# Performance work log

Hardware: AMD Instinct MI355X
Metric: run time of the kernel (lower is better)

The kernel has to match this reference:

```python
import jax, jax.numpy as jnp
import numpy as np

EPS = 1e-5
NUM_HEADS = 12

def _ln(x, g, b):
    m = jnp.mean(x, -1, keepdims=True)
    v = jnp.var(x, -1, keepdims=True)
    return (x - m) * jax.lax.rsqrt(v + EPS) * g + b

def setup_inputs():
    key = jax.random.key(0)
    ks = jax.random.split(key, 8)
    D, Dh = 768, 3072
    B, T, H, Wd = 8, 8, 14, 14
    def w(k, shape, scale=0.02):
        return jax.random.normal(k, shape, jnp.float32) * scale
    return dict(
        x=jax.random.normal(ks[0], (B, T * H * Wd + 1, D), jnp.float32),
        W_mq=w(ks[1], (D, D)), b_mq=jnp.zeros((D,), jnp.float32),
        W_mk=w(ks[2], (D, D)), b_mk=jnp.zeros((D,), jnp.float32),
        g1=jnp.ones((D,), jnp.float32), be1=jnp.zeros((D,), jnp.float32),
        W_qkv=w(ks[3], (3 * D, D)),
        W_proj=w(ks[4], (D, D)), b_proj=jnp.zeros((D,), jnp.float32),
        g2=jnp.ones((D,), jnp.float32), be2=jnp.zeros((D,), jnp.float32),
        W_fc1=w(ks[5], (Dh, D)), b_fc1=jnp.zeros((Dh,), jnp.float32),
        W_fc2=w(ks[6], (D, Dh)), b_fc2=jnp.zeros((D,), jnp.float32),
        B=B, T=T, H=H, Wd=Wd,
    )

def reference(x, W_mq, b_mq, W_mk, b_mk, g1, be1, W_qkv, W_proj, b_proj,
              g2, be2, W_fc1, b_fc1, W_fc2, b_fc2, B, T, H, Wd):
    D = x.shape[-1]
    nh = NUM_HEADS
    hd = D // nh
    res = x
    # cls token: (B,1,D) -> repeated per frame -> (B*T,1,D)
    cls = jnp.repeat(x[:, :1, :], T, axis=1).reshape(B * T, 1, D)
    # spatial tokens: 'b (h w t) m -> (b t) (h w) m'  (t is fastest-varying)
    xs = x[:, 1:, :].reshape(B, H * Wd, T, D).transpose(0, 2, 1, 3).reshape(B * T, H * Wd, D)
    xt = jnp.concatenate([cls, xs], axis=1)  # (BT, N=197, D)
    # learned QK-gated mask
    qm = xt @ W_mq.T + b_mq
    km = xt @ W_mk.T + b_mk
    lm = jnp.einsum('bnd,bmd->bnm', qm, km)
    lm = lm.at[:, 0, 0].set(100.0)  # force cls->cls gate open
    lm = jax.nn.sigmoid(lm)
    # attention (drop rates are 0; drop_path is identity at inference)
    xn = _ln(xt, g1, be1)
    BT, N = xt.shape[0], xt.shape[1]
    qkv = (xn @ W_qkv.T).reshape(BT, N, 3, nh, hd).transpose(2, 0, 3, 1, 4)
    q, k, v = qkv[0], qkv[1], qkv[2]  # (BT, nh, N, hd)
    attn = jax.nn.softmax(jnp.einsum('bhnd,bhmd->bhnm', q, k) * (hd ** -0.5), axis=-1)
    attn = attn * lm[:, None, :, :]  # gate attention probs with learned mask
    o = jnp.einsum('bhnm,bhmd->bhnd', attn, v).transpose(0, 2, 1, 3).reshape(BT, N, D)
    o = o @ W_proj.T + b_proj
    # gather cls back (mean over frames) and scatter tokens back
    cls_o = jnp.mean(o[:, 0, :].reshape(B, T, D), axis=1, keepdims=True)  # (B,1,D)
    xs_o = o[:, 1:, :].reshape(B, T, H * Wd, D).transpose(0, 2, 1, 3).reshape(B, H * Wd * T, D)
    y = res + jnp.concatenate([cls_o, xs_o], axis=1)
    # MLP
    h = _ln(y, g2, be2)
    h = jax.nn.gelu(h @ W_fc1.T + b_fc1, approximate=False)
    y = y + (h @ W_fc2.T + b_fc2)
    return (y, lm)
```

## Files before the change

kernel.cpp:

```cpp
#include <hip/hip_runtime.h>
#include <cstdint>

typedef _Float16 f16;
typedef f16 f16x2 __attribute__((ext_vector_type(2)));
typedef f16 f16x4 __attribute__((ext_vector_type(4)));
typedef f16 f16x8 __attribute__((ext_vector_type(8)));
typedef float f32x4 __attribute__((ext_vector_type(4)));

constexpr int D = 768;
constexpr int NTOK = 197;
constexpr int BT = 64;
constexpr int ROWS_A = BT * NTOK;
constexpr int SEQ = 1569;
constexpr int ROWS_Y = 8 * SEQ;
constexpr int DH = 3072;
constexpr int CW = 2304;
constexpr long Y_ELEMS = (long)ROWS_Y * D;

__device__ __forceinline__ void gload_lds16(const f16* g, f16* l) {
  __builtin_amdgcn_global_load_lds(
      (const __attribute__((address_space(1))) void*)g,
      (__attribute__((address_space(3))) void*)l, 16, 0, 0);
}

constexpr int DD4 = D * D / 4;
constexpr int QKV4 = CW * D / 4;
constexpr int FC4 = DH * D / 4;
constexpr int WQ_TOT = 3 * DD4 + QKV4 + 2 * FC4;

__global__ __launch_bounds__(256) void cvt_weights(
    const float* __restrict__ wmq_f, const float* __restrict__ wmk_f,
    const float* __restrict__ wqkv_f, const float* __restrict__ wproj_f,
    const float* __restrict__ wfc1_f, const float* __restrict__ wfc2_f,
    f16* __restrict__ wmqk, f16* __restrict__ wqkv, f16* __restrict__ wproj,
    f16* __restrict__ wfc1, f16* __restrict__ wfc2) {
  const int i = blockIdx.x * 256 + threadIdx.x;
  const float* src;
  f16* dst;
  int j;
  if (i < DD4) { src = wmq_f; dst = wmqk; j = i; }
  else if (i < 2 * DD4) { src = wmk_f; dst = wmqk + (size_t)D * D; j = i - DD4; }
  else if (i < 2 * DD4 + QKV4) { src = wqkv_f; dst = wqkv; j = i - 2 * DD4; }
  else if (i < 3 * DD4 + QKV4) { src = wproj_f; dst = wproj; j = i - 2 * DD4 - QKV4; }
  else if (i < 3 * DD4 + QKV4 + FC4) { src = wfc1_f; dst = wfc1; j = i - 3 * DD4 - QKV4; }
  else if (i < WQ_TOT) { src = wfc2_f; dst = wfc2; j = i - 3 * DD4 - QKV4 - FC4; }
  else return;
  const float4 v = *(const float4*)(src + (size_t)j * 4);
  f16x4 o = {(f16)v.x, (f16)v.y, (f16)v.z, (f16)v.w};
  *(f16x4*)(dst + (size_t)j * 4) = o;
}

__global__ __launch_bounds__(256) void concat2_f32(const float* __restrict__ a,
                                                   const float* __restrict__ b,
                                                   float* __restrict__ o, int n) {
  int i = blockIdx.x * 256 + threadIdx.x;
  if (i < n) o[i] = a[i];
  else if (i < 2 * n) o[i] = b[i - n];
}

__global__ __launch_bounds__(192) void build_xt_xn(
    const float* __restrict__ x, const float* __restrict__ g1,
    const float* __restrict__ be1, f16* __restrict__ xt, f16* __restrict__ xn) {
  const int rid = blockIdx.x;
  const int bt = rid / NTOK, n = rid % NTOK;
  const int b = bt >> 3, t = bt & 7;
  const int src = (n == 0) ? b * SEQ : b * SEQ + 1 + (n - 1) * 8 + t;
  const int tid = threadIdx.x, d0 = tid * 4;
  const float4 v = *(const float4*)(x + (size_t)src * D + d0);
  float s = v.x + v.y + v.z + v.w;
  float q = v.x * v.x + v.y * v.y + v.z * v.z + v.w * v.w;
  const int lane = tid & 63, wv = tid >> 6;
  for (int off = 32; off; off >>= 1) {
    s += __shfl_xor(s, off);
    q += __shfl_xor(q, off);
  }
  __shared__ float red[2][3];
  if (lane == 0) { red[0][wv] = s; red[1][wv] = q; }
  __syncthreads();
  s = red[0][0] + red[0][1] + red[0][2];
  q = red[1][0] + red[1][1] + red[1][2];
  const float mean = s * (1.f / 768.f);
  const float var = q * (1.f / 768.f) - mean * mean;
  const float rs = rsqrtf(var + 1e-5f);
  const size_t ob = (size_t)rid * D + d0;
  f16x4 xo = {(f16)v.x, (f16)v.y, (f16)v.z, (f16)v.w};
  *(f16x4*)(xt + ob) = xo;
  const float4 gv = *(const float4*)(g1 + d0);
  const float4 bv = *(const float4*)(be1 + d0);
  f16x4 no = {(f16)((v.x - mean) * rs * gv.x + bv.x),
              (f16)((v.y - mean) * rs * gv.y + bv.y),
              (f16)((v.z - mean) * rs * gv.z + bv.z),
              (f16)((v.w - mean) * rs * gv.w + bv.w)};
  *(f16x4*)(xn + ob) = no;
}

constexpr int EPI_F16 = 0;
constexpr int EPI_F16_BIAS = 1;
constexpr int EPI_SIG = 2;
constexpr int EPI_F16_BIAS_GELU = 3;
constexpr int EPI_F32_BIAS_RES = 4;

template <int EPI, int BNT = 128, int WPE = 3>
__global__ __launch_bounds__(256, WPE) void gemm_f16(
    const f16* __restrict__ A, const f16* __restrict__ B,
    const float* __restrict__ bias, float* __restrict__ Cf,
    f16* __restrict__ Ch, const float* __restrict__ Res, int M, int N, int K,
    int lda, int ldb, int ldc, long sA, long sB, long sC) {
  constexpr int BM = 128, BK = 32;
  constexpr int NJ = BNT / 32;
  __shared__ f16 As[2][BM][BK];
  __shared__ f16 Bs[2][BNT][BK];
  const int tid = threadIdx.x;
  const int bm = blockIdx.y * BM, bn = blockIdx.x * BNT;
  const int z = blockIdx.z;
  A += (size_t)z * sA;
  B += (size_t)z * sB;
  const int lane = tid & 63, wave = tid >> 6;
  const int wm = (wave >> 1) * 64, wn = (wave & 1) * (BNT / 2);
  const int l15 = lane & 15, quad = lane >> 4;

  const int gr = lane >> 2;
  const int gc = (lane & 3) * 8;
  int a_row0 = bm + wave * 16 + gr;       if (a_row0 >= M) a_row0 = M - 1;
  int a_row1 = bm + (wave + 4) * 16 + gr; if (a_row1 >= M) a_row1 = M - 1;
  int b_row0 = bn + wave * 16 + gr;       if (b_row0 >= N) b_row0 = N - 1;
  int b_row1 = bn + (wave + 4) * 16 + gr; if (b_row1 >= N) b_row1 = N - 1;
  const f16* ap0 = A + (size_t)a_row0 * lda + gc;
  const f16* ap1 = A + (size_t)a_row1 * lda + gc;
  const f16* bp0 = B + (size_t)b_row0 * ldb + gc;
  const f16* bp1 = B + (size_t)b_row1 * ldb + gc;

  f32x4 acc[4][NJ] = {};

  auto stage = [&](int buf, int k) {
    gload_lds16(ap0 + k, &As[buf][wave * 16][0]);
    gload_lds16(ap1 + k, &As[buf][(wave + 4) * 16][0]);
    gload_lds16(bp0 + k, &Bs[buf][wave * 16][0]);
    if constexpr (BNT == 128)
      gload_lds16(bp1 + k, &Bs[buf][(wave + 4) * 16][0]);
  };
  auto compute = [&](int buf) {
    f16x8 af[4], bf[NJ];
#pragma unroll
    for (int i = 0; i < 4; i++)
      af[i] = *(const f16x8*)&As[buf][wm + i * 16 + l15][quad * 8];
#pragma unroll
    for (int j = 0; j < NJ; j++)
      bf[j] = *(const f16x8*)&Bs[buf][wn + j * 16 + l15][quad * 8];
#pragma unroll
    for (int i = 0; i < 4; i++)
#pragma unroll
      for (int j = 0; j < NJ; j++)
        acc[i][j] =
            __builtin_amdgcn_mfma_f32_16x16x32_f16(af[i], bf[j], acc[i][j], 0, 0, 0);
  };

  stage(0, 0);
  __syncthreads();
  for (int kt = 0; kt < K; kt += 2 * BK) {
    stage(1, kt + BK);
    compute(0);
    __syncthreads();
    if (kt + 2 * BK < K) stage(0, kt + 2 * BK);
    compute(1);
    __syncthreads();
  }

#pragma unroll
  for (int i = 0; i < 4; i++) {
#pragma unroll
    for (int j = 0; j < NJ; j++) {
      const int col = bn + wn + j * 16 + l15;
      if (col >= N) continue;
#pragma unroll
      for (int r = 0; r < 4; r++) {
        const int row = bm + wm + i * 16 + quad * 4 + r;
        if (row >= M) continue;
        float v = acc[i][j][r];
        const size_t ci = (size_t)z * sC + (size_t)row * ldc + col;
        if constexpr (EPI == EPI_F16) {
          Ch[ci] = (f16)v;
        } else if constexpr (EPI == EPI_F16_BIAS) {
          Ch[ci] = (f16)(v + bias[col]);
        } else if constexpr (EPI == EPI_SIG) {
          if (row == 0 && col == 0) v = 100.f;
          Cf[ci] = 1.f / (1.f + __expf(-v));
        } else if constexpr (EPI == EPI_F16_BIAS_GELU) {
          const float u = v + bias[col];
          const float t = u * (0.79788456f + 0.0356774081f * u * u);
          const float e = __expf(2.f * t);
          Ch[ci] = (f16)(u * (e / (e + 1.f)));
        } else if constexpr (EPI == EPI_F32_BIAS_RES) {
          Cf[ci] = v + bias[col] + Res[ci];
        }
      }
    }
  }
}

__global__ __launch_bounds__(256, 2) void attn_kernel(
    const f16* __restrict__ qkv, const float* __restrict__ lm,
    f16* __restrict__ o) {
  __shared__ f16 Ks[208][72];
  __shared__ f16 Vt[64][232];
  __shared__ f16 Ps[4][16][40];
  const int bh = blockIdx.x;
  const int bt = bh / 12, h = bh % 12;
  const int tid = threadIdx.x, lane = tid & 63, w = tid >> 6;
  const int l15 = lane & 15, quad = lane >> 4;
  const size_t base = (size_t)bt * NTOK * CW + (size_t)h * 64;

  for (int idx = tid; idx < 208 * 8; idx += 256) {
    const int r = idx >> 3, c = (idx & 7) * 8;
    f16x8 kv = {};
    if (r < NTOK) kv = *(const f16x8*)(qkv + base + (size_t)r * CW + 768 + c);
    *(f16x8*)&Ks[r][c] = kv;
  }
  for (int cb = 0; cb < 8; cb++) {
    const int r = tid;
    if (r < NTOK) {
      const f16x8 vv = *(const f16x8*)(qkv + base + (size_t)r * CW + 1536 + cb * 8);
#pragma unroll
      for (int j = 0; j < 8; j++) Vt[cb * 8 + j][r] = vv[j];
    }
  }
  for (int idx = tid; idx < 64 * 35; idx += 256) {
    const int d = idx / 35, m = NTOK + idx % 35;
    Vt[d][m] = (f16)0.f;
  }
  __syncthreads();

  for (int nt = w; nt < 13; nt += 4) {
    const int nq = nt * 16 + l15;
    const f16* qrow = qkv + base + (size_t)nq * CW;
    const f16x8 aq0 = *(const f16x8*)(qrow + quad * 8);
    const f16x8 aq1 = *(const f16x8*)(qrow + 32 + quad * 8);
    f32x4 S[13];
#pragma unroll
    for (int t = 0; t < 13; t++) {
      const f16x8 bk0 = *(const f16x8*)&Ks[t * 16 + l15][quad * 8];
      const f16x8 bk1 = *(const f16x8*)&Ks[t * 16 + l15][32 + quad * 8];
      f32x4 s = {};
      s = __builtin_amdgcn_mfma_f32_16x16x32_f16(aq0, bk0, s, 0, 0, 0);
      s = __builtin_amdgcn_mfma_f32_16x16x32_f16(aq1, bk1, s, 0, 0, 0);
      S[t] = s;
    }
    float mx[4] = {-3e38f, -3e38f, -3e38f, -3e38f};
#pragma unroll
    for (int t = 0; t < 13; t++) {
      const int m = t * 16 + l15;
#pragma unroll
      for (int r = 0; r < 4; r++) {
        float v = (m < NTOK) ? S[t][r] * 0.125f : -1e30f;
        S[t][r] = v;
        mx[r] = fmaxf(mx[r], v);
      }
    }
#pragma unroll
    for (int off = 1; off < 16; off <<= 1)
#pragma unroll
      for (int r = 0; r < 4; r++) mx[r] = fmaxf(mx[r], __shfl_xor(mx[r], off));
    float den[4] = {0.f, 0.f, 0.f, 0.f};
#pragma unroll
    for (int t = 0; t < 13; t++)
#pragma unroll
      for (int r = 0; r < 4; r++) {
        const float e = __expf(S[t][r] - mx[r]);
        S[t][r] = e;
        den[r] += e;
      }
#pragma unroll
    for (int off = 1; off < 16; off <<= 1)
#pragma unroll
      for (int r = 0; r < 4; r++) den[r] += __shfl_xor(den[r], off);
    float inv[4];
#pragma unroll
    for (int r = 0; r < 4; r++) inv[r] = 1.f / den[r];
#pragma unroll
    for (int t = 0; t < 13; t++) {
      const int m = t * 16 + l15;
#pragma unroll
      for (int r = 0; r < 4; r++) {
        const int nrow = nt * 16 + quad * 4 + r;
        float g = 0.f;
        if (m < NTOK && nrow < NTOK)
          g = lm[((size_t)bt * NTOK + nrow) * NTOK + m];
        S[t][r] *= inv[r] * g;
      }
    }
    f32x4 O[4] = {};
    for (int c = 0; c < 7; c++) {
      __builtin_amdgcn_wave_barrier();
#pragma unroll
      for (int tt = 0; tt < 2; tt++) {
        const int t = 2 * c + tt;
#pragma unroll
        for (int r = 0; r < 4; r++) {
          const f16 pv = (t < 13) ? (f16)S[t][r] : (f16)0.f;
          Ps[w][quad * 4 + r][tt * 16 + l15] = pv;
        }
      }
      __builtin_amdgcn_wave_barrier();
      const f16x8 ap = *(const f16x8*)&Ps[w][l15][quad * 8];
#pragma unroll
      for (int dt = 0; dt < 4; dt++) {
        const f16x8 bv = *(const f16x8*)&Vt[dt * 16 + l15][c * 32 + quad * 8];
        O[dt] = __builtin_amdgcn_mfma_f32_16x16x32_f16(ap, bv, O[dt], 0, 0, 0);
      }
    }
#pragma unroll
    for (int dt = 0; dt < 4; dt++)
#pragma unroll
      for (int r = 0; r < 4; r++) {
        const int nrow = nt * 16 + quad * 4 + r;
        if (nrow < NTOK)
          o[((size_t)bt * NTOK + nrow) * D + h * 64 + dt * 16 + l15] =
              (f16)O[dt][r];
      }
  }
}

__global__ __launch_bounds__(192) void scatter_y_ln(
    const float* __restrict__ x, const f16* __restrict__ po,
    const float* __restrict__ g2, const float* __restrict__ be2,
    float* __restrict__ y, f16* __restrict__ yn) {
  const int rid = blockIdx.x;
  const int b = rid / SEQ, pos = rid % SEQ;
  const int tid = threadIdx.x, d0 = tid * 4;
  float4 v = *(const float4*)(x + (size_t)rid * D + d0);
  if (pos == 0) {
    float ax = 0, ay = 0, az = 0, aw = 0;
    for (int t = 0; t < 8; t++) {
      const f16x4 p = *(const f16x4*)(po + ((size_t)(b * 8 + t) * NTOK) * D + d0);
      ax += (float)p[0]; ay += (float)p[1]; az += (float)p[2]; aw += (float)p[3];
    }
    v.x += ax * 0.125f; v.y += ay * 0.125f; v.z += az * 0.125f; v.w += aw * 0.125f;
  } else {
    const int hw = (pos - 1) >> 3, t = (pos - 1) & 7;
    const f16x4 p =
        *(const f16x4*)(po + ((size_t)((b * 8 + t) * NTOK + 1 + hw)) * D + d0);
    v.x += (float)p[0]; v.y += (float)p[1]; v.z += (float)p[2]; v.w += (float)p[3];
  }
  *(float4*)(y + (size_t)rid * D + d0) = v;
  float s = v.x + v.y + v.z + v.w;
  float q = v.x * v.x + v.y * v.y + v.z * v.z + v.w * v.w;
  const int lane = tid & 63, wv = tid >> 6;
  for (int off = 32; off; off >>= 1) {
    s += __shfl_xor(s, off);
    q += __shfl_xor(q, off);
  }
  __shared__ float red[2][3];
  if (lane == 0) { red[0][wv] = s; red[1][wv] = q; }
  __syncthreads();
  s = red[0][0] + red[0][1] + red[0][2];
  q = red[1][0] + red[1][1] + red[1][2];
  const float mean = s * (1.f / 768.f);
  const float var = q * (1.f / 768.f) - mean * mean;
  const float rs = rsqrtf(var + 1e-5f);
  const float4 gv = *(const float4*)(g2 + d0);
  const float4 bv = *(const float4*)(be2 + d0);
  f16x4 no = {(f16)((v.x - mean) * rs * gv.x + bv.x),
              (f16)((v.y - mean) * rs * gv.y + bv.y),
              (f16)((v.z - mean) * rs * gv.z + bv.z),
              (f16)((v.w - mean) * rs * gv.w + bv.w)};
  *(f16x4*)(yn + (size_t)rid * D + d0) = no;
}

extern "C" void kernel_launch(void* const* d_in, const int* in_sizes, int n_in,
                              void* d_out, int out_size, void* d_ws,
                              size_t ws_size, hipStream_t stream) {
  const float* x = (const float*)d_in[0];
  const float* W_mq = (const float*)d_in[1];
  const float* b_mq = (const float*)d_in[2];
  const float* W_mk = (const float*)d_in[3];
  const float* b_mk = (const float*)d_in[4];
  const float* g1 = (const float*)d_in[5];
  const float* be1 = (const float*)d_in[6];
  const float* W_qkv = (const float*)d_in[7];
  const float* W_proj = (const float*)d_in[8];
  const float* b_proj = (const float*)d_in[9];
  const float* g2 = (const float*)d_in[10];
  const float* be2 = (const float*)d_in[11];
  const float* W_fc1 = (const float*)d_in[12];
  const float* b_fc1 = (const float*)d_in[13];
  const float* W_fc2 = (const float*)d_in[14];
  const float* b_fc2 = (const float*)d_in[15];

  char* ws = (char*)d_ws;
  size_t off = 0;
  auto alloc = [&](size_t bytes) {
    size_t o = off;
    off = (off + bytes + 255) & ~(size_t)255;
    return o;
  };
  const size_t o_wmqk = alloc((size_t)2 * D * D * 2);
  const size_t o_bmqk = alloc((size_t)2 * D * 4);
  const size_t o_wqkv = alloc((size_t)CW * D * 2);
  const size_t o_wproj = alloc((size_t)D * D * 2);
  const size_t o_wfc1 = alloc((size_t)DH * D * 2);
  const size_t o_wfc2 = alloc((size_t)D * DH * 2);
  const size_t o_xt = alloc((size_t)ROWS_A * D * 2);
  const size_t o_xn = alloc((size_t)ROWS_A * D * 2);
  const size_t o_big = alloc((size_t)ROWS_A * CW * 2);
  const size_t o_po = alloc((size_t)ROWS_A * D * 2);
  const size_t o_qmkm = o_big;
  const size_t o_qkv = o_big;
  const size_t o_o = o_xn;
  const size_t o_yn = o_xt;
  const size_t o_h = o_big;

  f16* wmqk = (f16*)(ws + o_wmqk);
  float* bmqk = (float*)(ws + o_bmqk);
  f16* wqkv = (f16*)(ws + o_wqkv);
  f16* wproj = (f16*)(ws + o_wproj);
  f16* wfc1 = (f16*)(ws + o_wfc1);
  f16* wfc2 = (f16*)(ws + o_wfc2);
  f16* xt = (f16*)(ws + o_xt);
  f16* xn = (f16*)(ws + o_xn);
  f16* qmkm = (f16*)(ws + o_qmkm);
  f16* qkv = (f16*)(ws + o_qkv);
  f16* oatt = (f16*)(ws + o_o);
  f16* po = (f16*)(ws + o_po);
  f16* yn = (f16*)(ws + o_yn);
  f16* h = (f16*)(ws + o_h);

  float* y_out = (float*)d_out;
  float* lm_out = (float*)d_out + Y_ELEMS;

  const dim3 blk(256);
  cvt_weights<<<dim3((WQ_TOT + 255) / 256), blk, 0, stream>>>(
      W_mq, W_mk, W_qkv, W_proj, W_fc1, W_fc2, wmqk, wqkv, wproj, wfc1, wfc2);
  concat2_f32<<<dim3(6), blk, 0, stream>>>(b_mq, b_mk, bmqk, D);

  build_xt_xn<<<dim3(ROWS_A), dim3(192), 0, stream>>>(x, g1, be1, xt, xn);

  auto grd = [](int N_, int M_, int Z_) {
    return dim3((N_ + 127) / 128, (M_ + 127) / 128, Z_);
  };
  auto grd64 = [](int N_, int M_) {
    return dim3((N_ + 63) / 64, (M_ + 127) / 128, 1);
  };
  gemm_f16<EPI_F16_BIAS><<<grd(2 * D, ROWS_A, 1), blk, 0, stream>>>(
      xt, wmqk, bmqk, nullptr, qmkm, nullptr, ROWS_A, 2 * D, D, D, D, 2 * D,
      0, 0, 0);
  gemm_f16<EPI_SIG><<<grd(NTOK, NTOK, BT), blk, 0, stream>>>(
      qmkm, qmkm + D, nullptr, lm_out, nullptr, nullptr, NTOK, NTOK, D,
      2 * D, 2 * D, NTOK, (long)NTOK * 2 * D, (long)NTOK * 2 * D,
      (long)NTOK * NTOK);
  gemm_f16<EPI_F16><<<grd(CW, ROWS_A, 1), blk, 0, stream>>>(
      xn, wqkv, nullptr, nullptr, qkv, nullptr, ROWS_A, CW, D, D, D, CW,
      0, 0, 0);
  attn_kernel<<<dim3(BT * 12), blk, 0, stream>>>(qkv, lm_out, oatt);
  gemm_f16<EPI_F16_BIAS, 64, 4><<<grd64(D, ROWS_A), blk, 0, stream>>>(
      oatt, wproj, b_proj, nullptr, po, nullptr, ROWS_A, D, D, D, D, D,
      0, 0, 0);
  scatter_y_ln<<<dim3(ROWS_Y), dim3(192), 0, stream>>>(x, po, g2, be2, y_out, yn);
  gemm_f16<EPI_F16_BIAS_GELU><<<grd(DH, ROWS_Y, 1), blk, 0, stream>>>(
      yn, wfc1, b_fc1, nullptr, h, nullptr, ROWS_Y, DH, D, D, D, DH, 0, 0, 0);
  gemm_f16<EPI_F32_BIAS_RES, 64, 4><<<grd64(D, ROWS_Y), blk, 0, stream>>>(
      h, wfc2, b_fc2, y_out, nullptr, y_out, ROWS_Y, D, DH, DH, DH, D,
      0, 0, 0);
  (void)in_sizes; (void)n_in; (void)out_size; (void)ws_size;
}
```

Baseline: 666.2 us.

## Fold mask Q/K projections into a single precomputed Wq^T Wk product

Rewrites the gated-mask logits as xt·(Wq^T Wk)·xt^T plus rank-one bias terms. A D×D combined weight is precomputed, and per-row bias dot products alpha and beta are computed inside the LayerNorm kernel. This replaces the 2D-wide projection GEMM with a D-wide one and adds the bias terms in the sigmoid epilogue. The GEMM template is also reshaped so the narrow variants tile 64 rows × 128 columns instead of 128×64, with occupancy hints raised. This changes fp16 rounding of the combined weight and adds small prep kernels.

```diff
diff --git a/kernel.cpp b/kernel.cpp
--- a/kernel.cpp
+++ b/kernel.cpp
@@ -26,59 +26,101 @@
 constexpr int DD4 = D * D / 4;
 constexpr int QKV4 = CW * D / 4;
 constexpr int FC4 = DH * D / 4;
-constexpr int WQ_TOT = 3 * DD4 + QKV4 + 2 * FC4;
+constexpr int W2_TOT = QKV4 + DD4 + 2 * FC4;
 
 __global__ __launch_bounds__(256) void cvt_weights(
-    const float* __restrict__ wmq_f, const float* __restrict__ wmk_f,
     const float* __restrict__ wqkv_f, const float* __restrict__ wproj_f,
     const float* __restrict__ wfc1_f, const float* __restrict__ wfc2_f,
-    f16* __restrict__ wmqk, f16* __restrict__ wqkv, f16* __restrict__ wproj,
+    f16* __restrict__ wqkv, f16* __restrict__ wproj,
     f16* __restrict__ wfc1, f16* __restrict__ wfc2) {
   const int i = blockIdx.x * 256 + threadIdx.x;
   const float* src;
   f16* dst;
   int j;
-  if (i < DD4) { src = wmq_f; dst = wmqk; j = i; }
-  else if (i < 2 * DD4) { src = wmk_f; dst = wmqk + (size_t)D * D; j = i - DD4; }
-  else if (i < 2 * DD4 + QKV4) { src = wqkv_f; dst = wqkv; j = i - 2 * DD4; }
-  else if (i < 3 * DD4 + QKV4) { src = wproj_f; dst = wproj; j = i - 2 * DD4 - QKV4; }
-  else if (i < 3 * DD4 + QKV4 + FC4) { src = wfc1_f; dst = wfc1; j = i - 3 * DD4 - QKV4; }
-  else if (i < WQ_TOT) { src = wfc2_f; dst = wfc2; j = i - 3 * DD4 - QKV4 - FC4; }
+  if (i < QKV4) { src = wqkv_f; dst = wqkv; j = i; }
+  else if (i < QKV4 + DD4) { src = wproj_f; dst = wproj; j = i - QKV4; }
+  else if (i < QKV4 + DD4 + FC4) { src = wfc1_f; dst = wfc1; j = i - QKV4 - DD4; }
+  else if (i < W2_TOT) { src = wfc2_f; dst = wfc2; j = i - QKV4 - DD4 - FC4; }
   else return;
   const float4 v = *(const float4*)(src + (size_t)j * 4);
   f16x4 o = {(f16)v.x, (f16)v.y, (f16)v.z, (f16)v.w};
   *(f16x4*)(dst + (size_t)j * 4) = o;
 }
 
-__global__ __launch_bounds__(256) void concat2_f32(const float* __restrict__ a,
-                                                   const float* __restrict__ b,
-                                                   float* __restrict__ o, int n) {
-  int i = blockIdx.x * 256 + threadIdx.x;
-  if (i < n) o[i] = a[i];
-  else if (i < 2 * n) o[i] = b[i - n];
+__global__ __launch_bounds__(256) void transpose2_f16(
+    const float* __restrict__ wq, const float* __restrict__ wk,
+    f16* __restrict__ wqT, f16* __restrict__ wkT) {
+  __shared__ float tile[32][33];
+  const int bid = blockIdx.x;
+  const int bx = bid % 24, by = (bid / 24) % 24, z = bid / 576;
+  const float* src = z ? wk : wq;
+  f16* dst = z ? wkT : wqT;
+  const int tx = threadIdx.x & 31, ty4 = (threadIdx.x >> 5) * 4;
+#pragma unroll
+  for (int r = 0; r < 4; r++)
+    tile[ty4 + r][tx] = src[(size_t)(by * 32 + ty4 + r) * D + bx * 32 + tx];
+  __syncthreads();
+#pragma unroll
+  for (int r = 0; r < 4; r++)
+    dst[(size_t)(bx * 32 + ty4 + r) * D + by * 32 + tx] = (f16)tile[tx][ty4 + r];
+}
+
+__global__ __launch_bounds__(256) void weight_prep(
+    const float* __restrict__ wq, const float* __restrict__ wk,
+    const float* __restrict__ bq, const float* __restrict__ bk,
+    float* __restrict__ rq, float* __restrict__ rk, float* __restrict__ beta) {
+  const int tid = blockIdx.x * 256 + threadIdx.x;
+  if (tid < D) {
+    float s = 0.f;
+    for (int k = 0; k < D; k++) s += wq[(size_t)k * D + tid] * bk[k];
+    rq[tid] = s;
+  } else if (tid < 2 * D) {
+    const int i = tid - D;
+    float s = 0.f;
+    for (int k = 0; k < D; k++) s += wk[(size_t)k * D + i] * bq[k];
+    rk[i] = s;
+  }
+  if (blockIdx.x == 0 && threadIdx.x < 64) {
+    float c = 0.f;
+    for (int k = threadIdx.x; k < D; k += 64) c += bq[k] * bk[k];
+    for (int off = 32; off; off >>= 1) c += __shfl_xor(c, off);
+    if (threadIdx.x == 0) beta[ROWS_A] = c;
+  }
 }
 
 __global__ __launch_bounds__(192) void build_xt_xn(
     const float* __restrict__ x, const float* __restrict__ g1,
-    const float* __restrict__ be1, f16* __restrict__ xt, f16* __restrict__ xn) {
+    const float* __restrict__ be1, const float* __restrict__ rq,
+    const float* __restrict__ rk, f16* __restrict__ xt, f16* __restrict__ xn,
+    float* __restrict__ alpha, float* __restrict__ beta) {
   const int rid = blockIdx.x;
   const int bt = rid / NTOK, n = rid % NTOK;
   const int b = bt >> 3, t = bt & 7;
   const int src = (n == 0) ? b * SEQ : b * SEQ + 1 + (n - 1) * 8 + t;
   const int tid = threadIdx.x, d0 = tid * 4;
   const float4 v = *(const float4*)(x + (size_t)src * D + d0);
+  const float4 rqv = *(const float4*)(rq + d0);
+  const float4 rkv = *(const float4*)(rk + d0);
   float s = v.x + v.y + v.z + v.w;
   float q = v.x * v.x + v.y * v.y + v.z * v.z + v.w * v.w;
+  float a = v.x * rqv.x + v.y * rqv.y + v.z * rqv.z + v.w * rqv.w;
+  float bb = v.x * rkv.x + v.y * rkv.y + v.z * rkv.z + v.w * rkv.w;
   const int lane = tid & 63, wv = tid >> 6;
   for (int off = 32; off; off >>= 1) {
     s += __shfl_xor(s, off);
     q += __shfl_xor(q, off);
-  }
-  __shared__ float red[2][3];
-  if (lane == 0) { red[0][wv] = s; red[1][wv] = q; }
+    a += __shfl_xor(a, off);
+    bb += __shfl_xor(bb, off);
+  }
+  __shared__ float red[4][3];
+  if (lane == 0) { red[0][wv] = s; red[1][wv] = q; red[2][wv] = a; red[3][wv] = bb; }
   __syncthreads();
   s = red[0][0] + red[0][1] + red[0][2];
   q = red[1][0] + red[1][1] + red[1][2];
+  if (tid == 0) {
+    alpha[rid] = red[2][0] + red[2][1] + red[2][2];
+    beta[rid] = red[3][0] + red[3][1] + red[3][2];
+  }
   const float mean = s * (1.f / 768.f);
   const float var = q * (1.f / 768.f) - mean * mean;
   const float rs = rsqrtf(var + 1e-5f);
@@ -100,23 +142,23 @@
 constexpr int EPI_F16_BIAS_GELU = 3;
 constexpr int EPI_F32_BIAS_RES = 4;
 
-template <int EPI, int BNT = 128, int WPE = 3>
-__global__ __launch_bounds__(256, WPE) void gemm_f16(
+template <int EPI, int BMT = 128, int MINW = 4>
+__global__ __launch_bounds__(256, MINW) void gemm_f16(
     const f16* __restrict__ A, const f16* __restrict__ B,
     const float* __restrict__ bias, float* __restrict__ Cf,
     f16* __restrict__ Ch, const float* __restrict__ Res, int M, int N, int K,
     int lda, int ldb, int ldc, long sA, long sB, long sC) {
-  constexpr int BM = 128, BK = 32;
-  constexpr int NJ = BNT / 32;
-  __shared__ f16 As[2][BM][BK];
-  __shared__ f16 Bs[2][BNT][BK];
+  constexpr int BN = 128, BK = 32;
+  constexpr int MI = (BMT / 2) / 16;
+  __shared__ f16 As[2][BMT][BK];
+  __shared__ f16 Bs[2][BN][BK];
   const int tid = threadIdx.x;
-  const int bm = blockIdx.y * BM, bn = blockIdx.x * BNT;
+  const int bm = blockIdx.y * BMT, bn = blockIdx.x * BN;
   const int z = blockIdx.z;
   A += (size_t)z * sA;
   B += (size_t)z * sB;
   const int lane = tid & 63, wave = tid >> 6;
-  const int wm = (wave >> 1) * 64, wn = (wave & 1) * (BNT / 2);
+  const int wm = (wave >> 1) * (BMT / 2), wn = (wave & 1) * 64;
   const int l15 = lane & 15, quad = lane >> 4;
 
   const int gr = lane >> 2;
@@ -130,27 +172,27 @@
   const f16* bp0 = B + (size_t)b_row0 * ldb + gc;
   const f16* bp1 = B + (size_t)b_row1 * ldb + gc;
 
-  f32x4 acc[4][NJ] = {};
+  f32x4 acc[MI][4] = {};
 
   auto stage = [&](int buf, int k) {
     gload_lds16(ap0 + k, &As[buf][wave * 16][0]);
-    gload_lds16(ap1 + k, &As[buf][(wave + 4) * 16][0]);
+    if constexpr (BMT == 128)
+      gload_lds16(ap1 + k, &As[buf][(wave + 4) * 16][0]);
     gload_lds16(bp0 + k, &Bs[buf][wave * 16][0]);
-    if constexpr (BNT == 128)
-      gload_lds16(bp1 + k, &Bs[buf][(wave + 4) * 16][0]);
+    gload_lds16(bp1 + k, &Bs[buf][(wave + 4) * 16][0]);
   };
   auto compute = [&](int buf) {
-    f16x8 af[4], bf[NJ];
-#pragma unroll
-    for (int i = 0; i < 4; i++)
+    f16x8 af[MI], bf[4];
+#pragma unroll
+    for (int i = 0; i < MI; i++)
       af[i] = *(const f16x8*)&As[buf][wm + i * 16 + l15][quad * 8];
 #pragma unroll
-    for (int j = 0; j < NJ; j++)
+    for (int j = 0; j < 4; j++)
       bf[j] = *(const f16x8*)&Bs[buf][wn + j * 16 + l15][quad * 8];
 #pragma unroll
-    for (int i = 0; i < 4; i++)
-#pragma unroll
-      for (int j = 0; j < NJ; j++)
+    for (int i = 0; i < MI; i++)
+#pragma unroll
+      for (int j = 0; j < 4; j++)
         acc[i][j] =
             __builtin_amdgcn_mfma_f32_16x16x32_f16(af[i], bf[j], acc[i][j], 0, 0, 0);
   };
@@ -167,9 +209,9 @@
   }
 
 #pragma unroll
-  for (int i = 0; i < 4; i++) {
-#pragma unroll
-    for (int j = 0; j < NJ; j++) {
+  for (int i = 0; i < MI; i++) {
+#pragma unroll
+    for (int j = 0; j < 4; j++) {
       const int col = bn + wn + j * 16 + l15;
       if (col >= N) continue;
 #pragma unroll
@@ -183,6 +225,8 @@
         } else if constexpr (EPI == EPI_F16_BIAS) {
           Ch[ci] = (f16)(v + bias[col]);
         } else if constexpr (EPI == EPI_SIG) {
+          v += bias[(size_t)z * NTOK + row] + Res[(size_t)z * NTOK + col] +
+               Res[ROWS_A];
           if (row == 0 && col == 0) v = 100.f;
           Cf[ci] = 1.f / (1.f + __expf(-v));
         } else if constexpr (EPI == EPI_F16_BIAS_GELU) {
@@ -393,8 +437,13 @@
     off = (off + bytes + 255) & ~(size_t)255;
     return o;
   };
-  const size_t o_wmqk = alloc((size_t)2 * D * D * 2);
-  const size_t o_bmqk = alloc((size_t)2 * D * 4);
+  const size_t o_wqT = alloc((size_t)D * D * 2);
+  const size_t o_wkT = alloc((size_t)D * D * 2);
+  const size_t o_wct = alloc((size_t)D * D * 2);
+  const size_t o_rq = alloc((size_t)D * 4);
+  const size_t o_rk = alloc((size_t)D * 4);
+  const size_t o_alpha = alloc((size_t)(ROWS_A + 1) * 4);
+  const size_t o_beta = alloc((size_t)(ROWS_A + 1) * 4);
   const size_t o_wqkv = alloc((size_t)CW * D * 2);
   const size_t o_wproj = alloc((size_t)D * D * 2);
   const size_t o_wfc1 = alloc((size_t)DH * D * 2);
@@ -403,21 +452,26 @@
   const size_t o_xn = alloc((size_t)ROWS_A * D * 2);
   const size_t o_big = alloc((size_t)ROWS_A * CW * 2);
   const size_t o_po = alloc((size_t)ROWS_A * D * 2);
-  const size_t o_qmkm = o_big;
+  const size_t o_t = o_po;
   const size_t o_qkv = o_big;
   const size_t o_o = o_xn;
   const size_t o_yn = o_xt;
   const size_t o_h = o_big;
 
-  f16* wmqk = (f16*)(ws + o_wmqk);
-  float* bmqk = (float*)(ws + o_bmqk);
+  f16* wqT = (f16*)(ws + o_wqT);
+  f16* wkT = (f16*)(ws + o_wkT);
+  f16* wct = (f16*)(ws + o_wct);
+  float* rq = (float*)(ws + o_rq);
+  float* rk = (float*)(ws + o_rk);
+  float* alpha = (float*)(ws + o_alpha);
+  float* beta = (float*)(ws + o_beta);
   f16* wqkv = (f16*)(ws + o_wqkv);
   f16* wproj = (f16*)(ws + o_wproj);
   f16* wfc1 = (f16*)(ws + o_wfc1);
   f16* wfc2 = (f16*)(ws + o_wfc2);
   f16* xt = (f16*)(ws + o_xt);
   f16* xn = (f16*)(ws + o_xn);
-  f16* qmkm = (f16*)(ws + o_qmkm);
+  f16* tmat = (f16*)(ws + o_t);
   f16* qkv = (f16*)(ws + o_qkv);
   f16* oatt = (f16*)(ws + o_o);
   f16* po = (f16*)(ws + o_po);
@@ -428,36 +482,39 @@
   float* lm_out = (float*)d_out + Y_ELEMS;
 
   const dim3 blk(256);
-  cvt_weights<<<dim3((WQ_TOT + 255) / 256), blk, 0, stream>>>(
-      W_mq, W_mk, W_qkv, W_proj, W_fc1, W_fc2, wmqk, wqkv, wproj, wfc1, wfc2);
-  concat2_f32<<<dim3(6), blk, 0, stream>>>(b_mq, b_mk, bmqk, D);
-
-  build_xt_xn<<<dim3(ROWS_A), dim3(192), 0, stream>>>(x, g1, be1, xt, xn);
+  cvt_weights<<<dim3((W2_TOT + 255) / 256), blk, 0, stream>>>(
+      W_qkv, W_proj, W_fc1, W_fc2, wqkv, wproj, wfc1, wfc2);
+  transpose2_f16<<<dim3(24 * 24 * 2), blk, 0, stream>>>(W_mq, W_mk, wqT, wkT);
+  weight_prep<<<dim3(6), blk, 0, stream>>>(W_mq, W_mk, b_mq, b_mk, rq, rk, beta);
+
+  build_xt_xn<<<dim3(ROWS_A), dim3(192), 0, stream>>>(x, g1, be1, rq, rk, xt,
+                                                      xn, alpha, beta);
 
   auto grd = [](int N_, int M_, int Z_) {
     return dim3((N_ + 127) / 128, (M_ + 127) / 128, Z_);
   };
-  auto grd64 = [](int N_, int M_) {
-    return dim3((N_ + 63) / 64, (M_ + 127) / 128, 1);
+  auto grd64 = [](int N_, int M_, int Z_) {
+    return dim3((N_ + 127) / 128, (M_ + 63) / 64, Z_);
   };
-  gemm_f16<EPI_F16_BIAS><<<grd(2 * D, ROWS_A, 1), blk, 0, stream>>>(
-      xt, wmqk, bmqk, nullptr, qmkm, nullptr, ROWS_A, 2 * D, D, D, D, 2 * D,
+  gemm_f16<EPI_F16><<<grd(D, D, 1), blk, 0, stream>>>(
+      wkT, wqT, nullptr, nullptr, wct, nullptr, D, D, D, D, D, D, 0, 0, 0);
+  gemm_f16<EPI_F16, 64, 5><<<grd64(D, ROWS_A, 1), blk, 0, stream>>>(
+      xt, wct, nullptr, nullptr, tmat, nullptr, ROWS_A, D, D, D, D, D,
       0, 0, 0);
-  gemm_f16<EPI_SIG><<<grd(NTOK, NTOK, BT), blk, 0, stream>>>(
-      qmkm, qmkm + D, nullptr, lm_out, nullptr, nullptr, NTOK, NTOK, D,
-      2 * D, 2 * D, NTOK, (long)NTOK * 2 * D, (long)NTOK * 2 * D,
-      (long)NTOK * NTOK);
+  gemm_f16<EPI_SIG, 64, 5><<<grd64(NTOK, NTOK, BT), blk, 0, stream>>>(
+      tmat, xt, alpha, lm_out, nullptr, beta, NTOK, NTOK, D, D, D, NTOK,
+      (long)NTOK * D, (long)NTOK * D, (long)NTOK * NTOK);
   gemm_f16<EPI_F16><<<grd(CW, ROWS_A, 1), blk, 0, stream>>>(
       xn, wqkv, nullptr, nullptr, qkv, nullptr, ROWS_A, CW, D, D, D, CW,
       0, 0, 0);
   attn_kernel<<<dim3(BT * 12), blk, 0, stream>>>(qkv, lm_out, oatt);
-  gemm_f16<EPI_F16_BIAS, 64, 4><<<grd64(D, ROWS_A), blk, 0, stream>>>(
+  gemm_f16<EPI_F16_BIAS, 64, 5><<<grd64(D, ROWS_A, 1), blk, 0, stream>>>(
       oatt, wproj, b_proj, nullptr, po, nullptr, ROWS_A, D, D, D, D, D,
       0, 0, 0);
   scatter_y_ln<<<dim3(ROWS_Y), dim3(192), 0, stream>>>(x, po, g2, be2, y_out, yn);
   gemm_f16<EPI_F16_BIAS_GELU><<<grd(DH, ROWS_Y, 1), blk, 0, stream>>>(
       yn, wfc1, b_fc1, nullptr, h, nullptr, ROWS_Y, DH, D, D, D, DH, 0, 0, 0);
-  gemm_f16<EPI_F32_BIAS_RES, 64, 4><<<grd64(D, ROWS_Y), blk, 0, stream>>>(
+  gemm_f16<EPI_F32_BIAS_RES, 64, 5><<<grd64(D, ROWS_Y, 1), blk, 0, stream>>>(
       h, wfc2, b_fc2, y_out, nullptr, y_out, ROWS_Y, D, DH, DH, DH, D,
       0, 0, 0);
   (void)in_sizes; (void)n_in; (void)out_size; (void)ws_size;
```

Result: slower. 698.3 us (+4.8%).
